# Optimization experiments

Measured on AMD Instinct MI355X. Metric: run time of the kernel, lower is better.

Reference implementation:

```python
import jax, jax.numpy as jnp
import numpy as np

ALPHA = 0.2  # LeakyReLU negative slope
MASK_FILL = -9e15


def setup_inputs() -> dict:
    key = jax.random.key(0)
    k_x, k_adj, k_W, k_a = jax.random.split(key, 4)
    B, N, Fin, T, O = 8, 1024, 64, 8, 128
    x = jax.random.normal(k_x, (B, N, Fin, T), dtype=jnp.float32)
    adj = (jax.random.uniform(k_adj, (N, N)) < 0.05).astype(jnp.float32)
    adj = jnp.maximum(adj, jnp.eye(N, dtype=jnp.float32))
    W = jax.random.normal(k_W, (Fin, O), dtype=jnp.float32) * (1.414 * (6.0 / (Fin + O)) ** 0.5)
    a = jax.random.normal(k_a, (2 * O, 1), dtype=jnp.float32) * (1.414 * (6.0 / (2 * O + 1)) ** 0.5)
    return {"x": x, "adj": adj, "W": W, "a": a}


def reference(x, adj, W, a):
    # x: (B, N, Fin, T), adj: (N, N), W: (Fin, O), a: (2O, 1)
    O = W.shape[1]
    xt = jnp.transpose(x, (0, 3, 1, 2))                 # (B, T, N, Fin)
    Wh = jnp.einsum('btnf,fo->btno', xt, W)             # (B, T, N, O)
    a1 = a[:O, 0]                                       # (O,)
    a2 = a[O:, 0]                                       # (O,)
    Wh1 = Wh @ a1                                       # (B, T, N)
    Wh2 = Wh @ a2                                       # (B, T, N)
    e = Wh1[..., :, None] + Wh2[..., None, :]           # (B, T, N, N): e_ij = Wh1_i + Wh2_j
    e = jax.nn.leaky_relu(e, negative_slope=ALPHA)
    e = jnp.where(adj > 0, e, MASK_FILL)
    attn = jax.nn.softmax(e, axis=-1)                   # softmax over neighbors j (torch dim=1 on (N,N))
    # dropout on attention is identity at inference (training=False)
    h_prime = jnp.einsum('btij,btjo->btio', attn, Wh)   # (B, T, N, O)
    out = jnp.transpose(h_prime, (0, 2, 3, 1))          # (B, N, O, T)
    return jax.nn.elu(out)                              # concat=True -> ELU
```

## Files before the change

kernel.cpp:

```cpp
#include <hip/hip_runtime.h>
#include <math.h>
#include <stdint.h>

#define ALPHA 0.2f

typedef __attribute__((ext_vector_type(8)))  short bf16x8;
typedef __attribute__((ext_vector_type(4)))  float f32x4;
typedef __attribute__((ext_vector_type(16))) float f32x16;

__device__ __forceinline__ uint32_t pack_bf16(float a, float b) {
    return ((__float_as_uint(a) + 0x8000u) >> 16) |
           ((__float_as_uint(b) + 0x8000u) & 0xFFFF0000u);
}

__global__ __launch_bounds__(512) void k_pre(const float* __restrict__ x,
                                             const float* __restrict__ W,
                                             const float* __restrict__ a,
                                             const float* __restrict__ adj,
                                             uint4* __restrict__ Whf,
                                             float* __restrict__ Wh1,
                                             float* __restrict__ Wh2,
                                             unsigned char* __restrict__ adjq) {
    __shared__ float xs[16 * 512];
    __shared__ float Wv[128 * 68];

    if (blockIdx.x >= 512) {
        int idx = (blockIdx.x - 512) * 512 + threadIdx.x;
        int i   = idx >> 7;
        int pos = idx & 127;
        const float4* a4 = (const float4*)adj + idx * 2;
        float4 v0 = a4[0], v1 = a4[1];
        unsigned int by = 0;
        by |= (v0.x > 0.f) ? 1u : 0u;
        by |= (v0.y > 0.f) ? 2u : 0u;
        by |= (v0.z > 0.f) ? 4u : 0u;
        by |= (v0.w > 0.f) ? 8u : 0u;
        by |= (v1.x > 0.f) ? 16u : 0u;
        by |= (v1.y > 0.f) ? 32u : 0u;
        by |= (v1.z > 0.f) ? 64u : 0u;
        by |= (v1.w > 0.f) ? 128u : 0u;
        adjq[(i << 7) + ((pos & 1) << 6) + (((pos >> 1) & 1) << 5) + (pos >> 2)] =
            (unsigned char)by;
        return;
    }

    const int tid = threadIdx.x;
    const int b   = blockIdx.x & 7;
    const int jt  = blockIdx.x >> 3;

    const float4* xg4 = (const float4*)(x + (size_t)(b * 1024 + jt * 16) * 512);
    #pragma unroll
    for (int i = 0; i < 4; ++i) {
        int    idx = tid + i * 512;
        float4 v   = xg4[idx];
        int jl  = idx >> 7;
        int rem = idx & 127;
        int f   = rem >> 1;
        int tq  = rem & 1;
        int kk  = f ^ ((jl >> 2) << 2);
        float* dst = &xs[jl * 512 + (tq * 4) * 64 + kk];
        dst[0]   = v.x;
        dst[64]  = v.y;
        dst[128] = v.z;
        dst[192] = v.w;
    }
    const float4* Wg4 = (const float4*)W;
    #pragma unroll
    for (int i = 0; i < 4; ++i) {
        int    idx = tid + i * 512;
        float4 v   = Wg4[idx];
        int k  = idx >> 5;
        int o0 = (idx & 31) * 4;
        #pragma unroll
        for (int c = 0; c < 4; ++c) {
            int o   = o0 + c;
            int adr = o * 68 + ((((k >> 2) ^ ((o >> 3) & 7)) << 2) | (k & 3));
            Wv[adr] = (&v.x)[c];
        }
    }
    __syncthreads();

    const int w  = tid >> 6;
    const int l  = tid & 63;
    const int q  = l >> 4;
    const int om = l & 15;
    const int t  = w;

    float acc[4][8];
    #pragma unroll
    for (int jj = 0; jj < 4; ++jj)
        #pragma unroll
        for (int nt = 0; nt < 8; ++nt) acc[jj][nt] = 0.f;

    for (int kc = 0; kc < 64; kc += 4) {
        float4 xv[4], wv[8];
        const int kx = kc ^ (q << 2);
        #pragma unroll
        for (int jj = 0; jj < 4; ++jj)
            xv[jj] = *(const float4*)&xs[(q * 4 + jj) * 512 + t * 64 + kx];
        #pragma unroll
        for (int nt = 0; nt < 8; ++nt) {
            int og  = nt * 16 + om;
            int grp = (kc >> 2) ^ ((nt * 2 + (om >> 3)) & 7);
            wv[nt]  = *(const float4*)&Wv[og * 68 + grp * 4];
        }
        #pragma unroll
        for (int jj = 0; jj < 4; ++jj) {
            #pragma unroll
            for (int nt = 0; nt < 8; ++nt) {
                float s = acc[jj][nt];
                s = fmaf(xv[jj].x, wv[nt].x, s);
                s = fmaf(xv[jj].y, wv[nt].y, s);
                s = fmaf(xv[jj].z, wv[nt].z, s);
                s = fmaf(xv[jj].w, wv[nt].w, s);
                acc[jj][nt] = s;
            }
        }
    }

    const int bt = b * 8 + t;

    float a1v[8], a2v[8];
    #pragma unroll
    for (int nt = 0; nt < 8; ++nt) {
        a1v[nt] = a[nt * 16 + om];
        a2v[nt] = a[128 + nt * 16 + om];
    }
    #pragma unroll
    for (int jj = 0; jj < 4; ++jj) {
        float s1 = 0.f, s2 = 0.f;
        #pragma unroll
        for (int nt = 0; nt < 8; ++nt) {
            s1 = fmaf(acc[jj][nt], a1v[nt], s1);
            s2 = fmaf(acc[jj][nt], a2v[nt], s2);
        }
        #pragma unroll
        for (int off = 1; off < 16; off <<= 1) {
            s1 += __shfl_xor(s1, off);
            s2 += __shfl_xor(s2, off);
        }
        if (om == 0) {
            int j = jt * 16 + q * 4 + jj;
            Wh1[bt * 1024 + j] = s1;
            Wh2[bt * 1024 + j] = s2;
        }
    }

    #pragma unroll
    for (int nt = 0; nt < 8; ++nt) {
        uint2 st;
        st.x = pack_bf16(acc[0][nt], acc[1][nt]);
        st.y = pack_bf16(acc[2][nt], acc[3][nt]);
        int    lane2 = ((q >> 1) << 5) | ((nt & 1) << 4) | om;
        size_t fidx  = ((size_t)(bt * 4 + (nt >> 1)) * 64 + jt) * 64 + lane2;
        char*  p     = (char*)(Whf + fidx) + ((q & 1) << 3);
        *(uint2*)p = st;
    }
}

__global__ __launch_bounds__(256) void k_agg(const uint4* __restrict__ Whf,
                                             const float* __restrict__ Wh1,
                                             const float* __restrict__ Wh2,
                                             const unsigned char* __restrict__ adjq,
                                             float* __restrict__ out) {
    __shared__ __attribute__((aligned(16))) uint4 bstage[2][1024];
    __shared__ __attribute__((aligned(16))) float efsE[1024];
    __shared__ __attribute__((aligned(16))) float efsF[1024];
    __shared__ float m2s[4];

    const int tid   = threadIdx.x;
    const int b     = blockIdx.x & 7;
    const int t     = (blockIdx.x >> 3) & 7;
    const int itile = blockIdx.x >> 6;
    const int bt    = b * 8 + t;
    const int i0    = itile * 128;

    const int w   = tid >> 6;
    const int l   = tid & 63;
    const int col = l & 31;
    const int g   = l >> 5;
    const int row = w * 32 + col;

    const uint4* plane = Whf + (size_t)bt * 16384;

    uint4 pf[4];
    #pragma unroll
    for (int f = 0; f < 4; ++f) pf[f] = plane[(w * 64 + f) * 64 + l];

    const uint4* ap = (const uint4*)(adjq + ((size_t)(i0 + row) << 7) + (g << 6));
    uint4 am[4];
    #pragma unroll
    for (int f = 0; f < 4; ++f) am[f] = ap[f];

    const float* wh2g = Wh2 + bt * 1024;
    float mx = -1e30f;
    #pragma unroll
    for (int rep = 0; rep < 4; ++rep) {
        int   j  = tid + rep * 256;
        float h2 = wh2g[j];
        efsE[j] = __expf(h2);
        efsF[j] = __expf(ALPHA * h2);
        mx = fmaxf(mx, h2);
    }
    #pragma unroll
    for (int off = 1; off < 64; off <<= 1) mx = fmaxf(mx, __shfl_xor(mx, off));
    if (l == 0) m2s[w] = mx;
    const float h1 = Wh1[bt * 1024 + i0 + row];

    #pragma unroll
    for (int f = 0; f < 4; ++f) bstage[0][(w * 4 + f) * 64 + l] = pf[f];
    __syncthreads();

    const float M2 = fmaxf(fmaxf(m2s[0], m2s[1]), fmaxf(m2s[2], m2s[3]));
    const float e0 = h1 + M2;
    const float mp = fmaxf(e0, ALPHA * e0);
    const float Af = __expf(h1 - mp);
    const float Bf = __expf(ALPHA * h1 - mp);

    f32x16 acc[4];
    #pragma unroll
    for (int nt2 = 0; nt2 < 4; ++nt2)
        #pragma unroll
        for (int r = 0; r < 16; ++r) acc[nt2][r] = 0.f;
    f32x16 accl;
    #pragma unroll
    for (int r = 0; r < 16; ++r) accl[r] = 0.f;

    bf16x8 ones;
    #pragma unroll
    for (int i = 0; i < 8; ++i) ones[i] = (short)0x3F80;

    #pragma unroll
    for (int v = 0; v < 16; ++v) {
        if (v + 1 < 16) {
            #pragma unroll
            for (int f = 0; f < 4; ++f)
                pf[f] = plane[(w * 64 + (v + 1) * 4 + f) * 64 + l];
        }

        #pragma unroll
        for (int ts = 0; ts < 4; ++ts) {
            const int jb = v * 64 + ts * 16 + g * 8;
            float4 E0 = *(const float4*)&efsE[jb];
            float4 E1 = *(const float4*)&efsE[jb + 4];
            float4 F0 = *(const float4*)&efsF[jb];
            float4 F1 = *(const float4*)&efsF[jb + 4];

            const int      pe = (ts & 1) * 32 + (v >> 1) * 4 + (v & 1) * 2 + (ts >> 1);
            const uint4    av = am[pe >> 4];
            const int      cc = (pe >> 2) & 3;
            const uint32_t cw = (cc == 0) ? av.x : (cc == 1) ? av.y
                               : (cc == 2) ? av.z : av.w;
            const uint32_t by = (cw >> ((pe & 3) * 8)) & 0xFFu;

            float p[8];
            p[0] = fmaxf(Af * E0.x, Bf * F0.x) * (float)((by >> 0) & 1u);
            p[1] = fmaxf(Af * E0.y, Bf * F0.y) * (float)((by >> 1) & 1u);
            p[2] = fmaxf(Af * E0.z, Bf * F0.z) * (float)((by >> 2) & 1u);
            p[3] = fmaxf(Af * E0.w, Bf * F0.w) * (float)((by >> 3) & 1u);
            p[4] = fmaxf(Af * E1.x, Bf * F1.x) * (float)((by >> 4) & 1u);
            p[5] = fmaxf(Af * E1.y, Bf * F1.y) * (float)((by >> 5) & 1u);
            p[6] = fmaxf(Af * E1.z, Bf * F1.z) * (float)((by >> 6) & 1u);
            p[7] = fmaxf(Af * E1.w, Bf * F1.w) * (float)((by >> 7) & 1u);

            union { uint32_t u32[4]; bf16x8 v8; } pk;
            #pragma unroll
            for (int r = 0; r < 4; ++r)
                pk.u32[r] = pack_bf16(p[2 * r], p[2 * r + 1]);

            #pragma unroll
            for (int nt2 = 0; nt2 < 4; ++nt2) {
                union { uint4 u4; bf16x8 v8; } br;
                br.u4 = bstage[v & 1][(nt2 * 4 + ts) * 64 + l];
                acc[nt2] = __builtin_amdgcn_mfma_f32_32x32x16_bf16(
                    pk.v8, br.v8, acc[nt2], 0, 0, 0);
            }
            accl = __builtin_amdgcn_mfma_f32_32x32x16_bf16(
                pk.v8, ones, accl, 0, 0, 0);
        }

        if (v + 1 < 16) {
            #pragma unroll
            for (int f = 0; f < 4; ++f)
                bstage[(v + 1) & 1][(w * 4 + f) * 64 + l] = pf[f];
        }
        __syncthreads();
    }

    float* og = out + ((size_t)(b * 1024 + i0 + w * 32)) * 1024 + t;
    #pragma unroll
    for (int reg = 0; reg < 16; ++reg) {
        const int   r    = (reg & 3) + 8 * (reg >> 2) + 4 * g;
        const float linv = 1.0f / accl[reg];
        #pragma unroll
        for (int nt2 = 0; nt2 < 4; ++nt2) {
            float vv = acc[nt2][reg] * linv;
            vv = vv > 0.f ? vv : __expf(vv) - 1.f;
            og[(size_t)r * 1024 + (nt2 * 32 + col) * 8] = vv;
        }
    }
}

extern "C" void kernel_launch(void* const* d_in, const int* in_sizes, int n_in,
                              void* d_out, int out_size, void* d_ws, size_t ws_size,
                              hipStream_t stream) {
    const float* x   = (const float*)d_in[0];
    const float* adj = (const float*)d_in[1];
    const float* W   = (const float*)d_in[2];
    const float* a   = (const float*)d_in[3];
    float* out = (float*)d_out;

    uint4*         Whf  = (uint4*)d_ws;
    float*         Wh1  = (float*)(Whf + 1048576);
    float*         Wh2  = Wh1 + 65536;
    unsigned char* adjq = (unsigned char*)(Wh2 + 65536);

    k_pre<<<768, 512, 0, stream>>>(x, W, a, adj, Whf, Wh1, Wh2, adjq);
    k_agg<<<512, 256, 0, stream>>>(Whf, Wh1, Wh2, adjq, out);
}
```

Before: 141.1 us.

## Split aggregation over j-halves per block and double grid size

Each k_agg block now covers 64 rows instead of 128. Its four waves split into two row groups times two halves of the neighbor dimension j, and the grid doubles to 1024 blocks. Partial accumulators are reduced across the j-halves through shared memory, with each half writing two of the four output column tiles. The intent is more blocks for better occupancy and load balance across CUs, paid for with extra shared-memory reduction traffic, more barriers, and twice the per-row setup work.

```diff
diff --git a/kernel.cpp b/kernel.cpp
--- a/kernel.cpp
+++ b/kernel.cpp
@@ -163,29 +163,32 @@
                                              const float* __restrict__ Wh2,
                                              const unsigned char* __restrict__ adjq,
                                              float* __restrict__ out) {
-    __shared__ __attribute__((aligned(16))) uint4 bstage[2][1024];
-    __shared__ __attribute__((aligned(16))) float efsE[1024];
-    __shared__ __attribute__((aligned(16))) float efsF[1024];
-    __shared__ float m2s[4];
+    __shared__ __attribute__((aligned(16))) uint4 bstage[2][2][4][64];
+    __shared__ __attribute__((aligned(16))) float efs[2][1024];
 
     const int tid   = threadIdx.x;
     const int b     = blockIdx.x & 7;
     const int t     = (blockIdx.x >> 3) & 7;
     const int itile = blockIdx.x >> 6;
     const int bt    = b * 8 + t;
-    const int i0    = itile * 128;
+    const int i0    = itile * 64;
 
     const int w   = tid >> 6;
     const int l   = tid & 63;
     const int col = l & 31;
     const int g   = l >> 5;
-    const int row = w * 32 + col;
+    const int jh  = w >> 1;
+    const int rg  = w & 1;
+    const int row = rg * 32 + col;
 
     const uint4* plane = Whf + (size_t)bt * 16384;
 
-    uint4 pf[4];
-    #pragma unroll
-    for (int f = 0; f < 4; ++f) pf[f] = plane[(w * 64 + f) * 64 + l];
+    float* m2sp = (float*)&bstage[1][0][0][0];
+
+    uint4 pf[2];
+    #pragma unroll
+    for (int jh2 = 0; jh2 < 2; ++jh2)
+        pf[jh2] = plane[(w * 64 + jh2 * 32 + 0) * 64 + l];
 
     const uint4* ap = (const uint4*)(adjq + ((size_t)(i0 + row) << 7) + (g << 6));
     uint4 am[4];
@@ -198,20 +201,23 @@
     for (int rep = 0; rep < 4; ++rep) {
         int   j  = tid + rep * 256;
         float h2 = wh2g[j];
-        efsE[j] = __expf(h2);
-        efsF[j] = __expf(ALPHA * h2);
+        efs[0][j] = __expf(h2);
+        efs[1][j] = __expf(ALPHA * h2);
         mx = fmaxf(mx, h2);
     }
     #pragma unroll
     for (int off = 1; off < 64; off <<= 1) mx = fmaxf(mx, __shfl_xor(mx, off));
-    if (l == 0) m2s[w] = mx;
+    if (l == 0) m2sp[w] = mx;
     const float h1 = Wh1[bt * 1024 + i0 + row];
 
     #pragma unroll
-    for (int f = 0; f < 4; ++f) bstage[0][(w * 4 + f) * 64 + l] = pf[f];
-    __syncthreads();
-
-    const float M2 = fmaxf(fmaxf(m2s[0], m2s[1]), fmaxf(m2s[2], m2s[3]));
+    for (int jh2 = 0; jh2 < 2; ++jh2)
+        bstage[0][jh2][w][l] = pf[jh2];
+    __syncthreads();
+
+    const float M2 = fmaxf(fmaxf(m2sp[0], m2sp[1]), fmaxf(m2sp[2], m2sp[3]));
+    __syncthreads();
+
     const float e0 = h1 + M2;
     const float mp = fmaxf(e0, ALPHA * e0);
     const float Af = __expf(h1 - mp);
@@ -231,22 +237,21 @@
     for (int i = 0; i < 8; ++i) ones[i] = (short)0x3F80;
 
     #pragma unroll
-    for (int v = 0; v < 16; ++v) {
-        if (v + 1 < 16) {
-            #pragma unroll
-            for (int f = 0; f < 4; ++f)
-                pf[f] = plane[(w * 64 + (v + 1) * 4 + f) * 64 + l];
-        }
-
-        #pragma unroll
-        for (int ts = 0; ts < 4; ++ts) {
-            const int jb = v * 64 + ts * 16 + g * 8;
-            float4 E0 = *(const float4*)&efsE[jb];
-            float4 E1 = *(const float4*)&efsE[jb + 4];
-            float4 F0 = *(const float4*)&efsF[jb];
-            float4 F1 = *(const float4*)&efsF[jb + 4];
-
-            const int      pe = (ts & 1) * 32 + (v >> 1) * 4 + (v & 1) * 2 + (ts >> 1);
+    for (int v = 0; v < 32; ++v) {
+        if (v + 1 < 32) {
+            #pragma unroll
+            for (int jh2 = 0; jh2 < 2; ++jh2)
+                pf[jh2] = plane[(w * 64 + jh2 * 32 + (v + 1)) * 64 + l];
+        }
+
+        {
+            const int jb = jh * 512 + v * 16 + g * 8;
+            float4 E0 = *(const float4*)&efs[0][jb];
+            float4 E1 = *(const float4*)&efs[0][jb + 4];
+            float4 F0 = *(const float4*)&efs[1][jb];
+            float4 F1 = *(const float4*)&efs[1][jb + 4];
+
+            const int      pe = (v & 1) * 32 + jh * 16 + (v >> 1);
             const uint4    av = am[pe >> 4];
             const int      cc = (pe >> 2) & 3;
             const uint32_t cw = (cc == 0) ? av.x : (cc == 1) ? av.y
@@ -271,7 +276,7 @@
             #pragma unroll
             for (int nt2 = 0; nt2 < 4; ++nt2) {
                 union { uint4 u4; bf16x8 v8; } br;
-                br.u4 = bstage[v & 1][(nt2 * 4 + ts) * 64 + l];
+                br.u4 = bstage[v & 1][jh][nt2][l];
                 acc[nt2] = __builtin_amdgcn_mfma_f32_32x32x16_bf16(
                     pk.v8, br.v8, acc[nt2], 0, 0, 0);
             }
@@ -279,21 +284,69 @@
                 pk.v8, ones, accl, 0, 0, 0);
         }
 
-        if (v + 1 < 16) {
-            #pragma unroll
-            for (int f = 0; f < 4; ++f)
-                bstage[(v + 1) & 1][(w * 4 + f) * 64 + l] = pf[f];
+        if (v + 1 < 32) {
+            #pragma unroll
+            for (int jh2 = 0; jh2 < 2; ++jh2)
+                bstage[(v + 1) & 1][jh2][w][l] = pf[jh2];
         }
         __syncthreads();
     }
 
-    float* og = out + ((size_t)(b * 1024 + i0 + w * 32)) * 1024 + t;
+    float* accw = (float*)bstage;
+    float* aclw = (float*)efs;
+
+    if (jh == 1) {
+        #pragma unroll
+        for (int k = 0; k < 2; ++k)
+            #pragma unroll
+            for (int r = 0; r < 16; ++r)
+                accw[(k * 16 + r) * 128 + rg * 64 + l] = acc[k][r];
+        #pragma unroll
+        for (int r = 0; r < 16; ++r)
+            aclw[r * 128 + rg * 64 + l] = accl[r];
+    }
+    __syncthreads();
+    if (jh == 0) {
+        #pragma unroll
+        for (int k = 0; k < 2; ++k)
+            #pragma unroll
+            for (int r = 0; r < 16; ++r)
+                acc[k][r] += accw[(k * 16 + r) * 128 + rg * 64 + l];
+        #pragma unroll
+        for (int r = 0; r < 16; ++r)
+            accl[r] += aclw[r * 128 + rg * 64 + l];
+    }
+    __syncthreads();
+    if (jh == 0) {
+        #pragma unroll
+        for (int k = 0; k < 2; ++k)
+            #pragma unroll
+            for (int r = 0; r < 16; ++r)
+                accw[(k * 16 + r) * 128 + rg * 64 + l] = acc[2 + k][r];
+        #pragma unroll
+        for (int r = 0; r < 16; ++r)
+            aclw[r * 128 + rg * 64 + l] = accl[r];
+    }
+    __syncthreads();
+    if (jh == 1) {
+        #pragma unroll
+        for (int k = 0; k < 2; ++k)
+            #pragma unroll
+            for (int r = 0; r < 16; ++r)
+                acc[2 + k][r] += accw[(k * 16 + r) * 128 + rg * 64 + l];
+        #pragma unroll
+        for (int r = 0; r < 16; ++r)
+            accl[r] = aclw[r * 128 + rg * 64 + l];
+    }
+
+    float* og = out + ((size_t)(b * 1024 + i0 + rg * 32)) * 1024 + t;
     #pragma unroll
     for (int reg = 0; reg < 16; ++reg) {
         const int   r    = (reg & 3) + 8 * (reg >> 2) + 4 * g;
         const float linv = 1.0f / accl[reg];
         #pragma unroll
-        for (int nt2 = 0; nt2 < 4; ++nt2) {
+        for (int k = 0; k < 2; ++k) {
+            const int nt2 = jh * 2 + k;
             float vv = acc[nt2][reg] * linv;
             vv = vv > 0.f ? vv : __expf(vv) - 1.f;
             og[(size_t)r * 1024 + (nt2 * 32 + col) * 8] = vv;
@@ -316,5 +369,5 @@
     unsigned char* adjq = (unsigned char*)(Wh2 + 65536);
 
     k_pre<<<768, 512, 0, stream>>>(x, W, a, adj, Whf, Wh1, Wh2, adjq);
-    k_agg<<<512, 256, 0, stream>>>(Whf, Wh1, Wh2, adjq, out);
+    k_agg<<<1024, 256, 0, stream>>>(Whf, Wh1, Wh2, adjq, out);
 }
```

Result: slower. 395.8 us (+180.6%).

## Halve k_agg block to two waves over 64 rows and single-buffer B staging

Applied to the files above, without the earlier changes.

The aggregation kernel now uses 128-thread blocks covering 64 rows each, so twice as many blocks (1024) launch, which should fill the CUs better. B-tile staging drops from double to single buffering with a sync on both sides of the store. The next prefetch is issued one step further ahead in registers, with each wave loading 8 uint4 per step. The extra barrier per step and the doubled Wh2/exp preprocessing and Whf plane loads across blocks may offset the gain.

```diff
diff --git a/kernel.cpp b/kernel.cpp
--- a/kernel.cpp
+++ b/kernel.cpp
@@ -158,34 +158,34 @@
     }
 }
 
-__global__ __launch_bounds__(256) void k_agg(const uint4* __restrict__ Whf,
+__global__ __launch_bounds__(128) void k_agg(const uint4* __restrict__ Whf,
                                              const float* __restrict__ Wh1,
                                              const float* __restrict__ Wh2,
                                              const unsigned char* __restrict__ adjq,
                                              float* __restrict__ out) {
-    __shared__ __attribute__((aligned(16))) uint4 bstage[2][1024];
-    __shared__ __attribute__((aligned(16))) float efsE[1024];
-    __shared__ __attribute__((aligned(16))) float efsF[1024];
-    __shared__ float m2s[4];
+    __shared__ __attribute__((aligned(16))) uint4 bstage[16][64];
+    __shared__ __attribute__((aligned(16))) float efs[2][1024];
+    __shared__ float m2s[2];
 
     const int tid   = threadIdx.x;
     const int b     = blockIdx.x & 7;
     const int t     = (blockIdx.x >> 3) & 7;
     const int itile = blockIdx.x >> 6;
     const int bt    = b * 8 + t;
-    const int i0    = itile * 128;
-
-    const int w   = tid >> 6;
+    const int i0    = itile * 64;
+
+    const int w2  = tid >> 6;
     const int l   = tid & 63;
     const int col = l & 31;
     const int g   = l >> 5;
-    const int row = w * 32 + col;
+    const int row = w2 * 32 + col;
 
     const uint4* plane = Whf + (size_t)bt * 16384;
 
-    uint4 pf[4];
-    #pragma unroll
-    for (int f = 0; f < 4; ++f) pf[f] = plane[(w * 64 + f) * 64 + l];
+    uint4 pf[8];
+    #pragma unroll
+    for (int f = 0; f < 8; ++f)
+        pf[f] = plane[((w2 * 2 + (f >> 2)) * 64 + (f & 3)) * 64 + l];
 
     const uint4* ap = (const uint4*)(adjq + ((size_t)(i0 + row) << 7) + (g << 6));
     uint4 am[4];
@@ -195,28 +195,33 @@
     const float* wh2g = Wh2 + bt * 1024;
     float mx = -1e30f;
     #pragma unroll
-    for (int rep = 0; rep < 4; ++rep) {
-        int   j  = tid + rep * 256;
+    for (int rep = 0; rep < 8; ++rep) {
+        int   j  = tid + rep * 128;
         float h2 = wh2g[j];
-        efsE[j] = __expf(h2);
-        efsF[j] = __expf(ALPHA * h2);
+        efs[0][j] = __expf(h2);
+        efs[1][j] = __expf(ALPHA * h2);
         mx = fmaxf(mx, h2);
     }
     #pragma unroll
     for (int off = 1; off < 64; off <<= 1) mx = fmaxf(mx, __shfl_xor(mx, off));
-    if (l == 0) m2s[w] = mx;
+    if (l == 0) m2s[w2] = mx;
     const float h1 = Wh1[bt * 1024 + i0 + row];
 
     #pragma unroll
-    for (int f = 0; f < 4; ++f) bstage[0][(w * 4 + f) * 64 + l] = pf[f];
+    for (int f = 0; f < 8; ++f)
+        bstage[(w2 * 2 + (f >> 2)) * 4 + (f & 3)][l] = pf[f];
     __syncthreads();
 
-    const float M2 = fmaxf(fmaxf(m2s[0], m2s[1]), fmaxf(m2s[2], m2s[3]));
+    const float M2 = fmaxf(m2s[0], m2s[1]);
     const float e0 = h1 + M2;
     const float mp = fmaxf(e0, ALPHA * e0);
     const float Af = __expf(h1 - mp);
     const float Bf = __expf(ALPHA * h1 - mp);
 
+    #pragma unroll
+    for (int f = 0; f < 8; ++f)
+        pf[f] = plane[((w2 * 2 + (f >> 2)) * 64 + 4 + (f & 3)) * 64 + l];
+
     f32x16 acc[4];
     #pragma unroll
     for (int nt2 = 0; nt2 < 4; ++nt2)
@@ -232,19 +237,13 @@
 
     #pragma unroll
     for (int v = 0; v < 16; ++v) {
-        if (v + 1 < 16) {
-            #pragma unroll
-            for (int f = 0; f < 4; ++f)
-                pf[f] = plane[(w * 64 + (v + 1) * 4 + f) * 64 + l];
-        }
-
         #pragma unroll
         for (int ts = 0; ts < 4; ++ts) {
             const int jb = v * 64 + ts * 16 + g * 8;
-            float4 E0 = *(const float4*)&efsE[jb];
-            float4 E1 = *(const float4*)&efsE[jb + 4];
-            float4 F0 = *(const float4*)&efsF[jb];
-            float4 F1 = *(const float4*)&efsF[jb + 4];
+            float4 E0 = *(const float4*)&efs[0][jb];
+            float4 E1 = *(const float4*)&efs[0][jb + 4];
+            float4 F0 = *(const float4*)&efs[1][jb];
+            float4 F1 = *(const float4*)&efs[1][jb + 4];
 
             const int      pe = (ts & 1) * 32 + (v >> 1) * 4 + (v & 1) * 2 + (ts >> 1);
             const uint4    av = am[pe >> 4];
@@ -271,7 +270,7 @@
             #pragma unroll
             for (int nt2 = 0; nt2 < 4; ++nt2) {
                 union { uint4 u4; bf16x8 v8; } br;
-                br.u4 = bstage[v & 1][(nt2 * 4 + ts) * 64 + l];
+                br.u4 = bstage[nt2 * 4 + ts][l];
                 acc[nt2] = __builtin_amdgcn_mfma_f32_32x32x16_bf16(
                     pk.v8, br.v8, acc[nt2], 0, 0, 0);
             }
@@ -279,15 +278,21 @@
                 pk.v8, ones, accl, 0, 0, 0);
         }
 
-        if (v + 1 < 16) {
+        if (v < 15) {
+            __syncthreads();
             #pragma unroll
-            for (int f = 0; f < 4; ++f)
-                bstage[(v + 1) & 1][(w * 4 + f) * 64 + l] = pf[f];
-        }
-        __syncthreads();
-    }
-
-    float* og = out + ((size_t)(b * 1024 + i0 + w * 32)) * 1024 + t;
+            for (int f = 0; f < 8; ++f)
+                bstage[(w2 * 2 + (f >> 2)) * 4 + (f & 3)][l] = pf[f];
+            __syncthreads();
+            if (v + 2 < 16) {
+                #pragma unroll
+                for (int f = 0; f < 8; ++f)
+                    pf[f] = plane[((w2 * 2 + (f >> 2)) * 64 + (v + 2) * 4 + (f & 3)) * 64 + l];
+            }
+        }
+    }
+
+    float* og = out + ((size_t)(b * 1024 + i0 + w2 * 32)) * 1024 + t;
     #pragma unroll
     for (int reg = 0; reg < 16; ++reg) {
         const int   r    = (reg & 3) + 8 * (reg >> 2) + 4 * g;
@@ -316,5 +321,5 @@
     unsigned char* adjq = (unsigned char*)(Wh2 + 65536);
 
     k_pre<<<768, 512, 0, stream>>>(x, W, a, adj, Whf, Wh1, Wh2, adjq);
-    k_agg<<<512, 256, 0, stream>>>(Whf, Wh1, Wh2, adjq, out);
+    k_agg<<<1024, 128, 0, stream>>>(Whf, Wh1, Wh2, adjq, out);
 }
```

Result: slower. 184.4 us (+30.7%).

## Compute Wh projection with bf16 MFMA instead of scalar FP32 FMAs

Applied to the files above, without the earlier changes.

The precompute kernel now converts x and W tiles to bf16 in swizzled shared memory and computes the projection with 32x32x16 bf16 MFMA instructions instead of FP32 FMA loops. The block layout changes to 256 threads handling 32 nodes by 4 time steps, and the adjacency-packing blocks are resized to match. Outputs are repacked with cross-lane shuffles into the existing Whf layout. Wh1/Wh2 are now computed from bf16-rounded inputs, which lowers precision of the attention logits.

```diff
diff --git a/kernel.cpp b/kernel.cpp
--- a/kernel.cpp
+++ b/kernel.cpp
@@ -12,8 +12,11 @@
     return ((__float_as_uint(a) + 0x8000u) >> 16) |
            ((__float_as_uint(b) + 0x8000u) & 0xFFFF0000u);
 }
-
-__global__ __launch_bounds__(512) void k_pre(const float* __restrict__ x,
+__device__ __forceinline__ unsigned short bf16_1(float a) {
+    return (unsigned short)((__float_as_uint(a) + 0x8000u) >> 16);
+}
+
+__global__ __launch_bounds__(256) void k_pre(const float* __restrict__ x,
                                              const float* __restrict__ W,
                                              const float* __restrict__ a,
                                              const float* __restrict__ adj,
@@ -21,11 +24,11 @@
                                              float* __restrict__ Wh1,
                                              float* __restrict__ Wh2,
                                              unsigned char* __restrict__ adjq) {
-    __shared__ float xs[16 * 512];
-    __shared__ float Wv[128 * 68];
+    __shared__ __attribute__((aligned(16))) unsigned short xbf[4 * 32 * 64];
+    __shared__ __attribute__((aligned(16))) unsigned short Wbf[128 * 64];
 
     if (blockIdx.x >= 512) {
-        int idx = (blockIdx.x - 512) * 512 + threadIdx.x;
+        int idx = (blockIdx.x - 512) * 256 + threadIdx.x;
         int i   = idx >> 7;
         int pos = idx & 127;
         const float4* a4 = (const float4*)adj + idx * 2;
@@ -44,117 +47,126 @@
         return;
     }
 
-    const int tid = threadIdx.x;
-    const int b   = blockIdx.x & 7;
-    const int jt  = blockIdx.x >> 3;
-
-    const float4* xg4 = (const float4*)(x + (size_t)(b * 1024 + jt * 16) * 512);
-    #pragma unroll
-    for (int i = 0; i < 4; ++i) {
-        int    idx = tid + i * 512;
-        float4 v   = xg4[idx];
-        int jl  = idx >> 7;
-        int rem = idx & 127;
-        int f   = rem >> 1;
-        int tq  = rem & 1;
-        int kk  = f ^ ((jl >> 2) << 2);
-        float* dst = &xs[jl * 512 + (tq * 4) * 64 + kk];
-        dst[0]   = v.x;
-        dst[64]  = v.y;
-        dst[128] = v.z;
-        dst[192] = v.w;
+    const int tid  = threadIdx.x;
+    const int b    = blockIdx.x & 7;
+    const int jt32 = (blockIdx.x >> 3) & 31;
+    const int th   = blockIdx.x >> 8;
+
+    const float* xg = x + ((size_t)(b * 1024 + jt32 * 32) * 64) * 8 + th * 4;
+    #pragma unroll
+    for (int i = 0; i < 8; ++i) {
+        int idx = tid + i * 256;
+        int j   = idx >> 6;
+        int f   = idx & 63;
+        float4 v = *(const float4*)(xg + (size_t)(j * 64 + f) * 8);
+        const int sw = ((j & 7) << 4);
+        *(unsigned short*)((char*)xbf + ((((0 * 32 + j) * 64 + f) * 2) ^ sw)) = bf16_1(v.x);
+        *(unsigned short*)((char*)xbf + ((((1 * 32 + j) * 64 + f) * 2) ^ sw)) = bf16_1(v.y);
+        *(unsigned short*)((char*)xbf + ((((2 * 32 + j) * 64 + f) * 2) ^ sw)) = bf16_1(v.z);
+        *(unsigned short*)((char*)xbf + ((((3 * 32 + j) * 64 + f) * 2) ^ sw)) = bf16_1(v.w);
     }
     const float4* Wg4 = (const float4*)W;
     #pragma unroll
-    for (int i = 0; i < 4; ++i) {
-        int    idx = tid + i * 512;
-        float4 v   = Wg4[idx];
-        int k  = idx >> 5;
-        int o0 = (idx & 31) * 4;
+    for (int i = 0; i < 8; ++i) {
+        int idx = tid + i * 256;
+        int fr  = idx >> 5;
+        int o0  = (idx & 31) * 4;
+        float4 v = Wg4[idx];
         #pragma unroll
         for (int c = 0; c < 4; ++c) {
-            int o   = o0 + c;
-            int adr = o * 68 + ((((k >> 2) ^ ((o >> 3) & 7)) << 2) | (k & 3));
-            Wv[adr] = (&v.x)[c];
+            int o = o0 + c;
+            *(unsigned short*)((char*)Wbf + (((o * 64 + fr) * 2) ^ ((o & 7) << 4))) =
+                bf16_1((&v.x)[c]);
         }
     }
     __syncthreads();
 
-    const int w  = tid >> 6;
-    const int l  = tid & 63;
-    const int q  = l >> 4;
-    const int om = l & 15;
-    const int t  = w;
-
-    float acc[4][8];
-    #pragma unroll
-    for (int jj = 0; jj < 4; ++jj)
-        #pragma unroll
-        for (int nt = 0; nt < 8; ++nt) acc[jj][nt] = 0.f;
-
-    for (int kc = 0; kc < 64; kc += 4) {
-        float4 xv[4], wv[8];
-        const int kx = kc ^ (q << 2);
-        #pragma unroll
-        for (int jj = 0; jj < 4; ++jj)
-            xv[jj] = *(const float4*)&xs[(q * 4 + jj) * 512 + t * 64 + kx];
-        #pragma unroll
-        for (int nt = 0; nt < 8; ++nt) {
-            int og  = nt * 16 + om;
-            int grp = (kc >> 2) ^ ((nt * 2 + (om >> 3)) & 7);
-            wv[nt]  = *(const float4*)&Wv[og * 68 + grp * 4];
-        }
-        #pragma unroll
-        for (int jj = 0; jj < 4; ++jj) {
-            #pragma unroll
-            for (int nt = 0; nt < 8; ++nt) {
-                float s = acc[jj][nt];
-                s = fmaf(xv[jj].x, wv[nt].x, s);
-                s = fmaf(xv[jj].y, wv[nt].y, s);
-                s = fmaf(xv[jj].z, wv[nt].z, s);
-                s = fmaf(xv[jj].w, wv[nt].w, s);
-                acc[jj][nt] = s;
-            }
-        }
-    }
-
-    const int bt = b * 8 + t;
-
-    float a1v[8], a2v[8];
-    #pragma unroll
-    for (int nt = 0; nt < 8; ++nt) {
-        a1v[nt] = a[nt * 16 + om];
-        a2v[nt] = a[128 + nt * 16 + om];
-    }
-    #pragma unroll
-    for (int jj = 0; jj < 4; ++jj) {
-        float s1 = 0.f, s2 = 0.f;
-        #pragma unroll
-        for (int nt = 0; nt < 8; ++nt) {
-            s1 = fmaf(acc[jj][nt], a1v[nt], s1);
-            s2 = fmaf(acc[jj][nt], a2v[nt], s2);
-        }
-        #pragma unroll
-        for (int off = 1; off < 16; off <<= 1) {
+    const int w   = tid >> 6;
+    const int l   = tid & 63;
+    const int col = l & 31;
+    const int g   = l >> 5;
+    const int t   = th * 4 + w;
+    const int bt  = b * 8 + t;
+
+    f32x16 acc[4];
+    #pragma unroll
+    for (int nt2 = 0; nt2 < 4; ++nt2)
+        #pragma unroll
+        for (int r = 0; r < 16; ++r) acc[nt2][r] = 0.f;
+
+    #pragma unroll
+    for (int kk = 0; kk < 4; ++kk) {
+        union { uint4 u4; bf16x8 v8; } av;
+        const int abyte = (((w * 32 + col) * 64 + kk * 16 + g * 8) * 2) ^ ((col & 7) << 4);
+        av.u4 = *(const uint4*)((const char*)xbf + abyte);
+        #pragma unroll
+        for (int nt2 = 0; nt2 < 4; ++nt2) {
+            union { uint4 u4; bf16x8 v8; } bv;
+            const int o     = nt2 * 32 + col;
+            const int bbyte = ((o * 64 + kk * 16 + g * 8) * 2) ^ ((o & 7) << 4);
+            bv.u4 = *(const uint4*)((const char*)Wbf + bbyte);
+            acc[nt2] = __builtin_amdgcn_mfma_f32_32x32x16_bf16(
+                av.v8, bv.v8, acc[nt2], 0, 0, 0);
+        }
+    }
+
+    float a1v[4], a2v[4];
+    #pragma unroll
+    for (int nt2 = 0; nt2 < 4; ++nt2) {
+        a1v[nt2] = a[nt2 * 32 + col];
+        a2v[nt2] = a[128 + nt2 * 32 + col];
+    }
+    #pragma unroll
+    for (int reg = 0; reg < 16; ++reg) {
+        float s1 = acc[0][reg] * a1v[0] + acc[1][reg] * a1v[1]
+                 + acc[2][reg] * a1v[2] + acc[3][reg] * a1v[3];
+        float s2 = acc[0][reg] * a2v[0] + acc[1][reg] * a2v[1]
+                 + acc[2][reg] * a2v[2] + acc[3][reg] * a2v[3];
+        #pragma unroll
+        for (int off = 1; off < 32; off <<= 1) {
             s1 += __shfl_xor(s1, off);
             s2 += __shfl_xor(s2, off);
         }
-        if (om == 0) {
-            int j = jt * 16 + q * 4 + jj;
+        if (col == 0) {
+            int j = jt32 * 32 + (reg & 3) + 8 * (reg >> 2) + 4 * g;
             Wh1[bt * 1024 + j] = s1;
             Wh2[bt * 1024 + j] = s2;
         }
     }
 
     #pragma unroll
-    for (int nt = 0; nt < 8; ++nt) {
-        uint2 st;
-        st.x = pack_bf16(acc[0][nt], acc[1][nt]);
-        st.y = pack_bf16(acc[2][nt], acc[3][nt]);
-        int    lane2 = ((q >> 1) << 5) | ((nt & 1) << 4) | om;
-        size_t fidx  = ((size_t)(bt * 4 + (nt >> 1)) * 64 + jt) * 64 + lane2;
-        char*  p     = (char*)(Whf + fidx) + ((q & 1) << 3);
-        *(uint2*)p = st;
+    for (int nt2 = 0; nt2 < 4; ++nt2) {
+        const uint32_t pk0 = pack_bf16(acc[nt2][0],  acc[nt2][1]);
+        const uint32_t pk1 = pack_bf16(acc[nt2][2],  acc[nt2][3]);
+        const uint32_t pk2 = pack_bf16(acc[nt2][4],  acc[nt2][5]);
+        const uint32_t pk3 = pack_bf16(acc[nt2][6],  acc[nt2][7]);
+        const uint32_t pk4 = pack_bf16(acc[nt2][8],  acc[nt2][9]);
+        const uint32_t pk5 = pack_bf16(acc[nt2][10], acc[nt2][11]);
+        const uint32_t pk6 = pack_bf16(acc[nt2][12], acc[nt2][13]);
+        const uint32_t pk7 = pack_bf16(acc[nt2][14], acc[nt2][15]);
+        const uint32_t xp0 = __shfl_xor(pk0, 32);
+        const uint32_t xp1 = __shfl_xor(pk1, 32);
+        const uint32_t xp2 = __shfl_xor(pk2, 32);
+        const uint32_t xp3 = __shfl_xor(pk3, 32);
+        const uint32_t xp4 = __shfl_xor(pk4, 32);
+        const uint32_t xp5 = __shfl_xor(pk5, 32);
+        const uint32_t xp6 = __shfl_xor(pk6, 32);
+        const uint32_t xp7 = __shfl_xor(pk7, 32);
+        const bool gh = (g != 0);
+
+        uint4 s0, s1q;
+        s0.x  = gh ? xp2 : pk0;
+        s0.y  = gh ? xp3 : pk1;
+        s0.z  = gh ? pk2 : xp0;
+        s0.w  = gh ? pk3 : xp1;
+        s1q.x = gh ? xp6 : pk4;
+        s1q.y = gh ? xp7 : pk5;
+        s1q.z = gh ? pk6 : xp4;
+        s1q.w = gh ? pk7 : xp5;
+
+        const size_t base = ((size_t)(bt * 4 + nt2) * 64 + jt32 * 2) * 64 + l;
+        Whf[base]      = s0;
+        Whf[base + 64] = s1q;
     }
 }
 
@@ -315,6 +327,6 @@
     float*         Wh2  = Wh1 + 65536;
     unsigned char* adjq = (unsigned char*)(Wh2 + 65536);
 
-    k_pre<<<768, 512, 0, stream>>>(x, W, a, adj, Whf, Wh1, Wh2, adjq);
+    k_pre<<<1024, 256, 0, stream>>>(x, W, a, adj, Whf, Wh1, Wh2, adjq);
     k_agg<<<512, 256, 0, stream>>>(Whf, Wh1, Wh2, adjq, out);
 }
```

After: 135.1 us. 4.2% less time.
